# Optimization experiments

Measured on AMD Instinct MI355X. Metric: run time of the kernel, lower is better.

The kernel has to match this reference:

```python
import jax, jax.numpy as jnp
import numpy as np

B, T, C = 2, 4096, 768
NH = 12
HD = C // NH  # 64


def setup_inputs() -> dict:
    key = jax.random.key(0)
    k0, k1, k2, k3, k4 = jax.random.split(key, 5)
    x = jax.random.normal(k0, (B, T, C), dtype=jnp.float32)
    # parameters (stored as [in, out] for x @ W)
    w_attn = jax.random.normal(k1, (C, 3 * C), dtype=jnp.float32) * 0.02
    b_attn = jnp.zeros((3 * C,), dtype=jnp.float32)
    w_proj = jax.random.normal(k2, (C, C), dtype=jnp.float32) * 0.02
    b_proj = jnp.zeros((C,), dtype=jnp.float32)
    return {"x": x, "w_attn": w_attn, "b_attn": b_attn, "w_proj": w_proj, "b_proj": b_proj}


def reference(x, w_attn, b_attn, w_proj, b_proj):
    Bv, Tv, Cv = x.shape
    qkv = x @ w_attn + b_attn  # (B,T,3C)
    q, k, v = jnp.split(qkv, 3, axis=2)
    # (B, NH, T, HD)
    q = q.reshape(Bv, Tv, NH, HD).transpose(0, 2, 1, 3)
    k = k.reshape(Bv, Tv, NH, HD).transpose(0, 2, 1, 3)
    v = v.reshape(Bv, Tv, NH, HD).transpose(0, 2, 1, 3)
    att = jnp.einsum('bhqd,bhkd->bhqk', q, k) / jnp.sqrt(jnp.float32(HD))
    causal = jnp.tril(jnp.ones((Tv, Tv), dtype=bool))  # mask buffer slice
    att = jnp.where(causal[None, None, :, :], att, jnp.float32(-jnp.inf))
    att = jax.nn.softmax(att, axis=-1)
    y = jnp.einsum('bhqk,bhkd->bhqd', att, v)
    y = y.transpose(0, 2, 1, 3).reshape(Bv, Tv, Cv)
    y = y @ w_proj + b_proj
    return y
```

## Files before the change

kernel.cpp:

```cpp
#include <hip/hip_runtime.h>

typedef __bf16 bf16;
typedef float f32x4 __attribute__((ext_vector_type(4)));
typedef bf16 bf16x8v __attribute__((ext_vector_type(8)));

#define MFMA_BF16(a, b, c) __builtin_amdgcn_mfma_f32_16x16x32_bf16((a), (b), (c), 0, 0, 0)

__device__ __forceinline__ void async16(const bf16* g, bf16* l) {
  __builtin_amdgcn_global_load_lds(
      (const __attribute__((address_space(1))) void*)g,
      (__attribute__((address_space(3))) void*)l, 16, 0, 0);
}

__global__ __launch_bounds__(256) void convert_kernel(
    const float* __restrict__ in, bf16* __restrict__ out, int n8) {
  int i = blockIdx.x * 256 + threadIdx.x;
  if (i >= n8) return;
  const float4* p = (const float4*)in + (size_t)i * 2;
  float4 a = p[0], b = p[1];
  bf16x8v o;
  o[0] = (bf16)a.x; o[1] = (bf16)a.y; o[2] = (bf16)a.z; o[3] = (bf16)a.w;
  o[4] = (bf16)b.x; o[5] = (bf16)b.y; o[6] = (bf16)b.z; o[7] = (bf16)b.w;
  ((bf16x8v*)out)[i] = o;
}

__global__ __launch_bounds__(256) void transpose_conv_kernel(
    const float* __restrict__ in, bf16* __restrict__ out, int R, int Ccols) {
  __shared__ float tile[32][33];
  int c0 = blockIdx.x * 32, r0 = blockIdx.y * 32;
  int tx = threadIdx.x & 31;
  int ty = threadIdx.x >> 5;
#pragma unroll
  for (int i = 0; i < 4; ++i) {
    int r = ty + i * 8;
    tile[r][tx] = in[(size_t)(r0 + r) * Ccols + c0 + tx];
  }
  __syncthreads();
#pragma unroll
  for (int i = 0; i < 4; ++i) {
    int c = ty + i * 8;
    out[(size_t)(c0 + c) * R + r0 + tx] = (bf16)tile[tx][c];
  }
}

__global__ __launch_bounds__(256) void transpose_bf16_kernel(
    const bf16* __restrict__ in, bf16* __restrict__ out, int R, int Ccols) {
  __shared__ bf16 tile[32][33];
  const bf16* inp = in + (size_t)blockIdx.z * R * Ccols;
  bf16* outp = out + (size_t)blockIdx.z * R * Ccols;
  int c0 = blockIdx.x * 32, r0 = blockIdx.y * 32;
  int tx = threadIdx.x & 31;
  int ty = threadIdx.x >> 5;
#pragma unroll
  for (int i = 0; i < 4; ++i) {
    int r = ty + i * 8;
    tile[r][tx] = inp[(size_t)(r0 + r) * Ccols + c0 + tx];
  }
  __syncthreads();
#pragma unroll
  for (int i = 0; i < 4; ++i) {
    int c = ty + i * 8;
    outp[(size_t)(c0 + c) * R + r0 + tx] = tile[tx][c];
  }
}

template <int MODE>
__global__ __launch_bounds__(256) void gemm_kernel(
    const bf16* __restrict__ A, const bf16* __restrict__ Bt,
    const float* __restrict__ bias, int N, float* __restrict__ outf,
    bf16* __restrict__ qo, bf16* __restrict__ ko, bf16* __restrict__ vo) {
  constexpr int Kdim = 768;
  __shared__ __align__(16) bf16 As[128][32];
  __shared__ __align__(16) bf16 Bs[128][32];
  const int tid = threadIdx.x;
  const int lane = tid & 63;
  const int wave = tid >> 6;
  const int wm = (wave >> 1) * 64, wn = (wave & 1) * 64;
  const int m0 = blockIdx.y * 128, n0 = blockIdx.x * 128;
  const int l15 = lane & 15, q4 = lane >> 4;

  f32x4 acc[4][4] = {};

  const int ca = wave * 2;
  const int ar = lane >> 2;
  const int ac = (lane & 3) * 8;
  bf16* asBase = &As[0][0];
  bf16* bsBase = &Bs[0][0];

  for (int k0 = 0; k0 < Kdim; k0 += 32) {
    const bf16* gA = A + (size_t)(m0 + ca * 16 + ar) * Kdim + k0 + ac;
    async16(gA, asBase + ca * 512);
    async16(gA + 16 * Kdim, asBase + (ca + 1) * 512);
    const bf16* gB = Bt + (size_t)(n0 + ca * 16 + ar) * Kdim + k0 + ac;
    async16(gB, bsBase + ca * 512);
    async16(gB + 16 * Kdim, bsBase + (ca + 1) * 512);
    __syncthreads();
    bf16x8v af[4], bfg[4];
#pragma unroll
    for (int i = 0; i < 4; ++i)
      af[i] = *(const bf16x8v*)&As[wm + i * 16 + l15][q4 * 8];
#pragma unroll
    for (int i = 0; i < 4; ++i)
      bfg[i] = *(const bf16x8v*)&Bs[wn + i * 16 + l15][q4 * 8];
#pragma unroll
    for (int mi = 0; mi < 4; ++mi)
#pragma unroll
      for (int ni = 0; ni < 4; ++ni)
        acc[mi][ni] = MFMA_BF16(af[mi], bfg[ni], acc[mi][ni]);
    __syncthreads();
  }

#pragma unroll
  for (int mi = 0; mi < 4; ++mi) {
#pragma unroll
    for (int ni = 0; ni < 4; ++ni) {
      int col = n0 + wn + ni * 16 + l15;
      float bv = bias[col];
#pragma unroll
      for (int r = 0; r < 4; ++r) {
        int row = m0 + wm + mi * 16 + q4 * 4 + r;
        float val = acc[mi][ni][r] + bv;
        if (MODE == 0) {
          outf[(size_t)row * N + col] = val;
        } else {
          int sel = col / 768;
          int cc = col - sel * 768;
          int h = cc >> 6, d = cc & 63;
          int b = row >> 12, t = row & 4095;
          bf16* dst = sel == 0 ? qo : (sel == 1 ? ko : vo);
          dst[((size_t)(b * 12 + h) * 4096 + t) * 64 + d] = (bf16)val;
        }
      }
    }
  }
}

__global__ __launch_bounds__(256, 3) void attn_kernel(
    const bf16* __restrict__ q, const bf16* __restrict__ k,
    const bf16* __restrict__ vt, bf16* __restrict__ y) {
  __shared__ __align__(16) bf16 Kb[2][64][64];
  __shared__ __align__(16) bf16 Vb[2][64][64];
  __shared__ __align__(16) bf16 Ps[4][32][64];
  const int tid = threadIdx.x;
  const int lane = tid & 63, wave = tid >> 6;
  const int l15 = lane & 15, q4 = lane >> 4;
  const int swz = l15 & 7;
  const int id = blockIdx.x;
  const int bh = id % 24;
  const int p = id / 24;
  const int myT = (wave < 2) ? (63 - p) : p;
  const int rs0 = myT * 64 + (wave & 1) * 32;
  const int rs1 = rs0 + 16;
  const int hb = bh % 12, bb = bh / 12;

  const int gr = lane >> 3;
  const int sj = (lane & 7) ^ gr;
  const bf16* kgbase = k + (size_t)bh * 4096 * 64;
  const bf16* vgbase = vt + (size_t)bh * 64 * 4096;

  bf16x8v ones;
#pragma unroll
  for (int j = 0; j < 8; ++j) ones[j] = (bf16)1.0f;

  bf16x8v qf[2][2];
#pragma unroll
  for (int st = 0; st < 2; ++st) {
    const bf16* qrow =
        q + ((size_t)bh * 4096 + rs0 + st * 16 + l15) * 64 + q4 * 8;
#pragma unroll
    for (int ks = 0; ks < 2; ++ks) {
      bf16x8v t8 = *(const bf16x8v*)(qrow + ks * 32);
#pragma unroll
      for (int j = 0; j < 8; ++j) t8[j] = (bf16)((float)t8[j] * 0.18033688f);
      qf[st][ks] = t8;
    }
  }

  f32x4 o0[4] = {}, o1[4] = {};
  f32x4 ol0 = {}, ol1 = {};

  auto stage = [&](int kt, int buf) {
    const int t0k = kt * 64;
#pragma unroll
    for (int g = 0; g < 2; ++g) {
      const int grp = wave * 2 + g;
      async16(kgbase + (size_t)(t0k + grp * 8 + gr) * 64 + sj * 8,
              &Kb[buf][grp * 8][0]);
      async16(vgbase + (size_t)(grp * 8 + gr) * 4096 + t0k + sj * 8,
              &Vb[buf][grp * 8][0]);
    }
  };

  const int ktmax = 64 - p;
  stage(0, 0);

  for (int kt = 0; kt < ktmax; ++kt) {
    const int buf = kt & 1;
    __syncthreads();
    if (kt + 1 < ktmax) stage(kt + 1, buf ^ 1);
    const int t0 = kt * 64;

    if (t0 <= rs1 + 15) {
      f32x4 s0[4] = {}, s1[4] = {};
#pragma unroll
      for (int ni = 0; ni < 4; ++ni) {
#pragma unroll
        for (int ks = 0; ks < 2; ++ks) {
          bf16x8v kf = *(const bf16x8v*)&Kb[buf][ni * 16 + l15]
                                           [((ks * 4 + q4) ^ swz) * 8];
          s0[ni] = MFMA_BF16(qf[0][ks], kf, s0[ni]);
          s1[ni] = MFMA_BF16(qf[1][ks], kf, s1[ni]);
        }
      }
      if (t0 + 63 <= rs1) {
#pragma unroll
        for (int ni = 0; ni < 4; ++ni) {
          const int jb = ni * 2 + (l15 >> 3);
#pragma unroll
          for (int r = 0; r < 4; ++r) {
            const int row = q4 * 4 + r;
            Ps[wave][16 + row][((jb ^ (row & 7)) * 8) + (l15 & 7)] =
                (bf16)__builtin_amdgcn_exp2f(s1[ni][r] - 28.8539008f);
          }
        }
      } else {
#pragma unroll
        for (int ni = 0; ni < 4; ++ni) {
          const int jb = ni * 2 + (l15 >> 3);
#pragma unroll
          for (int r = 0; r < 4; ++r) {
            float pv = (t0 + ni * 16 + l15 <= rs1 + q4 * 4 + r)
                           ? __builtin_amdgcn_exp2f(s1[ni][r] - 28.8539008f)
                           : 0.0f;
            const int row = q4 * 4 + r;
            Ps[wave][16 + row][((jb ^ (row & 7)) * 8) + (l15 & 7)] = (bf16)pv;
          }
        }
      }
      if (t0 + 63 <= rs0) {
#pragma unroll
        for (int ni = 0; ni < 4; ++ni) {
          const int jb = ni * 2 + (l15 >> 3);
#pragma unroll
          for (int r = 0; r < 4; ++r) {
            const int row = q4 * 4 + r;
            Ps[wave][row][((jb ^ (row & 7)) * 8) + (l15 & 7)] =
                (bf16)__builtin_amdgcn_exp2f(s0[ni][r] - 28.8539008f);
          }
        }
      } else {
#pragma unroll
        for (int ni = 0; ni < 4; ++ni) {
          const int jb = ni * 2 + (l15 >> 3);
#pragma unroll
          for (int r = 0; r < 4; ++r) {
            float pv = (t0 + ni * 16 + l15 <= rs0 + q4 * 4 + r)
                           ? __builtin_amdgcn_exp2f(s0[ni][r] - 28.8539008f)
                           : 0.0f;
            const int row = q4 * 4 + r;
            Ps[wave][row][((jb ^ (row & 7)) * 8) + (l15 & 7)] = (bf16)pv;
          }
        }
      }
      bf16x8v pf0[2], pf1[2];
#pragma unroll
      for (int ks = 0; ks < 2; ++ks) {
        pf1[ks] = *(const bf16x8v*)&Ps[wave][16 + l15]
                                      [((ks * 4 + q4) ^ swz) * 8];
        pf0[ks] = *(const bf16x8v*)&Ps[wave][l15][((ks * 4 + q4) ^ swz) * 8];
      }
#pragma unroll
      for (int d4 = 0; d4 < 4; ++d4) {
#pragma unroll
        for (int ks = 0; ks < 2; ++ks) {
          bf16x8v vf = *(const bf16x8v*)&Vb[buf][d4 * 16 + l15]
                                           [((ks * 4 + q4) ^ swz) * 8];
          o1[d4] = MFMA_BF16(pf1[ks], vf, o1[d4]);
          o0[d4] = MFMA_BF16(pf0[ks], vf, o0[d4]);
        }
      }
#pragma unroll
      for (int ks = 0; ks < 2; ++ks) {
        ol1 = MFMA_BF16(pf1[ks], ones, ol1);
        ol0 = MFMA_BF16(pf0[ks], ones, ol0);
      }
    }
  }

#pragma unroll
  for (int d4 = 0; d4 < 4; ++d4)
#pragma unroll
    for (int r = 0; r < 4; ++r) {
      int row0 = rs0 + q4 * 4 + r;
      y[((size_t)(bb * 4096 + row0)) * 768 + hb * 64 + d4 * 16 + l15] =
          (bf16)(o0[d4][r] / ol0[r]);
      int row1 = rs1 + q4 * 4 + r;
      y[((size_t)(bb * 4096 + row1)) * 768 + hb * 64 + d4 * 16 + l15] =
          (bf16)(o1[d4][r] / ol1[r]);
    }
}

extern "C" void kernel_launch(void* const* d_in, const int* in_sizes, int n_in,
                              void* d_out, int out_size, void* d_ws,
                              size_t ws_size, hipStream_t stream) {
  const float* x = (const float*)d_in[0];
  const float* w_attn = (const float*)d_in[1];
  const float* b_attn = (const float*)d_in[2];
  const float* w_proj = (const float*)d_in[3];
  const float* b_proj = (const float*)d_in[4];
  float* out = (float*)d_out;

  char* ws = (char*)d_ws;
  size_t off = 0;
  auto carve = [&](size_t elems) {
    char* p = ws + off;
    off += ((elems * sizeof(bf16) + 255) & ~(size_t)255);
    return (bf16*)p;
  };
  bf16* xb = carve((size_t)8192 * 768);
  bf16* wt_attn = carve((size_t)2304 * 768);
  bf16* wt_proj = carve((size_t)768 * 768);
  bf16* qb = carve((size_t)24 * 4096 * 64);
  bf16* kb = carve((size_t)24 * 4096 * 64);
  bf16* vb = carve((size_t)24 * 4096 * 64);
  bf16* vtb = xb;
  bf16* yb = vb;

  convert_kernel<<<(8192 * 768 / 8 + 255) / 256, 256, 0, stream>>>(
      x, xb, 8192 * 768 / 8);
  transpose_conv_kernel<<<dim3(2304 / 32, 768 / 32), 256, 0, stream>>>(
      w_attn, wt_attn, 768, 2304);
  transpose_conv_kernel<<<dim3(768 / 32, 768 / 32), 256, 0, stream>>>(
      w_proj, wt_proj, 768, 768);
  gemm_kernel<1><<<dim3(2304 / 128, 8192 / 128), 256, 0, stream>>>(
      xb, wt_attn, b_attn, 2304, nullptr, qb, kb, vb);
  transpose_bf16_kernel<<<dim3(64 / 32, 4096 / 32, 24), 256, 0, stream>>>(
      vb, vtb, 4096, 64);
  attn_kernel<<<dim3(768), 256, 0, stream>>>(qb, kb, vtb, yb);
  gemm_kernel<0><<<dim3(768 / 128, 8192 / 128), 256, 0, stream>>>(
      yb, wt_proj, b_proj, 768, out, nullptr, nullptr, nullptr);
}
```

Measured before the change: 257.9 us.

## Balance causal work per wave and transpose QK MFMA for vectorized P stores

Before, the two waves on the high query tile did all the work while the two waves on the low tile sat idle once past the diagonal. Now each wave holds one 16-row slice from the high tile and one from the low tile, so every wave does the same amount of causal work. The QK^T MFMA operands are swapped so each lane holds consecutive key columns, which lets P be written to LDS as 4-wide bf16 vectors instead of scalar stores. s_setprio hints are also added around the MFMA blocks, at the cost of more branching on the per-slice active flag.

```diff
diff --git a/kernel.cpp b/kernel.cpp
--- a/kernel.cpp
+++ b/kernel.cpp
@@ -3,6 +3,7 @@
 typedef __bf16 bf16;
 typedef float f32x4 __attribute__((ext_vector_type(4)));
 typedef bf16 bf16x8v __attribute__((ext_vector_type(8)));
+typedef bf16 bf16x4v __attribute__((ext_vector_type(4)));
 
 #define MFMA_BF16(a, b, c) __builtin_amdgcn_mfma_f32_16x16x32_bf16((a), (b), (c), 0, 0, 0)
 
@@ -148,9 +149,8 @@
   const int id = blockIdx.x;
   const int bh = id % 24;
   const int p = id / 24;
-  const int myT = (wave < 2) ? (63 - p) : p;
-  const int rs0 = myT * 64 + (wave & 1) * 32;
-  const int rs1 = rs0 + 16;
+  const int rs0 = (63 - p) * 64 + wave * 16;
+  const int rs1 = p * 64 + wave * 16;
   const int hb = bh % 12, bb = bh / 12;
 
   const int gr = lane >> 3;
@@ -165,8 +165,8 @@
   bf16x8v qf[2][2];
 #pragma unroll
   for (int st = 0; st < 2; ++st) {
-    const bf16* qrow =
-        q + ((size_t)bh * 4096 + rs0 + st * 16 + l15) * 64 + q4 * 8;
+    const int rs = st ? rs1 : rs0;
+    const bf16* qrow = q + ((size_t)bh * 4096 + rs + l15) * 64 + q4 * 8;
 #pragma unroll
     for (int ks = 0; ks < 2; ++ks) {
       bf16x8v t8 = *(const bf16x8v*)(qrow + ks * 32);
@@ -191,6 +191,33 @@
     }
   };
 
+  auto sm_full = [&](f32x4 (&s)[4]) {
+#pragma unroll
+    for (int ni = 0; ni < 4; ++ni)
+#pragma unroll
+      for (int r = 0; r < 4; ++r)
+        s[ni][r] = __builtin_amdgcn_exp2f(s[ni][r] - 28.8539008f);
+  };
+  auto sm_mask = [&](f32x4 (&s)[4], int lim) {
+#pragma unroll
+    for (int ni = 0; ni < 4; ++ni)
+#pragma unroll
+      for (int r = 0; r < 4; ++r)
+        s[ni][r] = (ni * 16 + q4 * 4 + r <= lim)
+                       ? __builtin_amdgcn_exp2f(s[ni][r] - 28.8539008f)
+                       : 0.0f;
+  };
+  auto pwrite = [&](const f32x4 (&s)[4], int row) {
+#pragma unroll
+    for (int ni = 0; ni < 4; ++ni) {
+      bf16x4v pv4;
+#pragma unroll
+      for (int e = 0; e < 4; ++e) pv4[e] = (bf16)s[ni][e];
+      const int jb = ni * 2 + (q4 >> 1);
+      *(bf16x4v*)&Ps[wave][row][((jb ^ (row & 7)) * 8) + (q4 & 1) * 4] = pv4;
+    }
+  };
+
   const int ktmax = 64 - p;
   stage(0, 0);
 
@@ -199,91 +226,81 @@
     __syncthreads();
     if (kt + 1 < ktmax) stage(kt + 1, buf ^ 1);
     const int t0 = kt * 64;
-
-    if (t0 <= rs1 + 15) {
-      f32x4 s0[4] = {}, s1[4] = {};
+    const bool act1 = (t0 <= rs1 + 15);
+
+    f32x4 s0[4] = {}, s1[4] = {};
+    __builtin_amdgcn_s_setprio(1);
+    if (act1) {
 #pragma unroll
       for (int ni = 0; ni < 4; ++ni) {
 #pragma unroll
         for (int ks = 0; ks < 2; ++ks) {
           bf16x8v kf = *(const bf16x8v*)&Kb[buf][ni * 16 + l15]
                                            [((ks * 4 + q4) ^ swz) * 8];
-          s0[ni] = MFMA_BF16(qf[0][ks], kf, s0[ni]);
-          s1[ni] = MFMA_BF16(qf[1][ks], kf, s1[ni]);
-        }
-      }
-      if (t0 + 63 <= rs1) {
-#pragma unroll
-        for (int ni = 0; ni < 4; ++ni) {
-          const int jb = ni * 2 + (l15 >> 3);
-#pragma unroll
-          for (int r = 0; r < 4; ++r) {
-            const int row = q4 * 4 + r;
-            Ps[wave][16 + row][((jb ^ (row & 7)) * 8) + (l15 & 7)] =
-                (bf16)__builtin_amdgcn_exp2f(s1[ni][r] - 28.8539008f);
-          }
-        }
-      } else {
-#pragma unroll
-        for (int ni = 0; ni < 4; ++ni) {
-          const int jb = ni * 2 + (l15 >> 3);
-#pragma unroll
-          for (int r = 0; r < 4; ++r) {
-            float pv = (t0 + ni * 16 + l15 <= rs1 + q4 * 4 + r)
-                           ? __builtin_amdgcn_exp2f(s1[ni][r] - 28.8539008f)
-                           : 0.0f;
-            const int row = q4 * 4 + r;
-            Ps[wave][16 + row][((jb ^ (row & 7)) * 8) + (l15 & 7)] = (bf16)pv;
-          }
-        }
-      }
-      if (t0 + 63 <= rs0) {
-#pragma unroll
-        for (int ni = 0; ni < 4; ++ni) {
-          const int jb = ni * 2 + (l15 >> 3);
-#pragma unroll
-          for (int r = 0; r < 4; ++r) {
-            const int row = q4 * 4 + r;
-            Ps[wave][row][((jb ^ (row & 7)) * 8) + (l15 & 7)] =
-                (bf16)__builtin_amdgcn_exp2f(s0[ni][r] - 28.8539008f);
-          }
-        }
-      } else {
-#pragma unroll
-        for (int ni = 0; ni < 4; ++ni) {
-          const int jb = ni * 2 + (l15 >> 3);
-#pragma unroll
-          for (int r = 0; r < 4; ++r) {
-            float pv = (t0 + ni * 16 + l15 <= rs0 + q4 * 4 + r)
-                           ? __builtin_amdgcn_exp2f(s0[ni][r] - 28.8539008f)
-                           : 0.0f;
-            const int row = q4 * 4 + r;
-            Ps[wave][row][((jb ^ (row & 7)) * 8) + (l15 & 7)] = (bf16)pv;
-          }
-        }
-      }
-      bf16x8v pf0[2], pf1[2];
-#pragma unroll
-      for (int ks = 0; ks < 2; ++ks) {
-        pf1[ks] = *(const bf16x8v*)&Ps[wave][16 + l15]
-                                      [((ks * 4 + q4) ^ swz) * 8];
-        pf0[ks] = *(const bf16x8v*)&Ps[wave][l15][((ks * 4 + q4) ^ swz) * 8];
-      }
+          s0[ni] = MFMA_BF16(kf, qf[0][ks], s0[ni]);
+          s1[ni] = MFMA_BF16(kf, qf[1][ks], s1[ni]);
+        }
+      }
+    } else {
+#pragma unroll
+      for (int ni = 0; ni < 4; ++ni) {
+#pragma unroll
+        for (int ks = 0; ks < 2; ++ks) {
+          bf16x8v kf = *(const bf16x8v*)&Kb[buf][ni * 16 + l15]
+                                           [((ks * 4 + q4) ^ swz) * 8];
+          s0[ni] = MFMA_BF16(kf, qf[0][ks], s0[ni]);
+        }
+      }
+    }
+    __builtin_amdgcn_s_setprio(0);
+
+    if (t0 + 63 <= rs0) sm_full(s0); else sm_mask(s0, rs0 + l15 - t0);
+    pwrite(s0, l15);
+    if (act1) {
+      if (t0 + 63 <= rs1) sm_full(s1); else sm_mask(s1, rs1 + l15 - t0);
+      pwrite(s1, 16 + l15);
+    }
+
+    bf16x8v pf0[2], pf1[2];
+#pragma unroll
+    for (int ks = 0; ks < 2; ++ks)
+      pf0[ks] = *(const bf16x8v*)&Ps[wave][l15][((ks * 4 + q4) ^ swz) * 8];
+    if (act1) {
+#pragma unroll
+      for (int ks = 0; ks < 2; ++ks)
+        pf1[ks] =
+            *(const bf16x8v*)&Ps[wave][16 + l15][((ks * 4 + q4) ^ swz) * 8];
+      __builtin_amdgcn_s_setprio(1);
 #pragma unroll
       for (int d4 = 0; d4 < 4; ++d4) {
 #pragma unroll
         for (int ks = 0; ks < 2; ++ks) {
           bf16x8v vf = *(const bf16x8v*)&Vb[buf][d4 * 16 + l15]
                                            [((ks * 4 + q4) ^ swz) * 8];
+          o0[d4] = MFMA_BF16(pf0[ks], vf, o0[d4]);
           o1[d4] = MFMA_BF16(pf1[ks], vf, o1[d4]);
+        }
+      }
+#pragma unroll
+      for (int ks = 0; ks < 2; ++ks) {
+        ol0 = MFMA_BF16(pf0[ks], ones, ol0);
+        ol1 = MFMA_BF16(pf1[ks], ones, ol1);
+      }
+      __builtin_amdgcn_s_setprio(0);
+    } else {
+      __builtin_amdgcn_s_setprio(1);
+#pragma unroll
+      for (int d4 = 0; d4 < 4; ++d4) {
+#pragma unroll
+        for (int ks = 0; ks < 2; ++ks) {
+          bf16x8v vf = *(const bf16x8v*)&Vb[buf][d4 * 16 + l15]
+                                           [((ks * 4 + q4) ^ swz) * 8];
           o0[d4] = MFMA_BF16(pf0[ks], vf, o0[d4]);
         }
       }
 #pragma unroll
-      for (int ks = 0; ks < 2; ++ks) {
-        ol1 = MFMA_BF16(pf1[ks], ones, ol1);
-        ol0 = MFMA_BF16(pf0[ks], ones, ol0);
-      }
+      for (int ks = 0; ks < 2; ++ks) ol0 = MFMA_BF16(pf0[ks], ones, ol0);
+      __builtin_amdgcn_s_setprio(0);
     }
   }
 
```

New measurement: 240.6 us. -6.7%, faster.
